# Optimization experiments

Measured on AMD Instinct MI355X. Metric: run time of the kernel, lower is better.

## Reference

```python
import jax, jax.numpy as jnp
import numpy as np

CAPACITY_FACTOR = 1.0


def setup_inputs() -> dict:
    key = jax.random.key(0)
    k1, k2, k3 = jax.random.split(key, 3)
    x = jax.random.normal(k1, (4, 2048, 2048), jnp.float32)          # [B, S, d_model]
    wg = jax.random.normal(k2, (2048, 8), jnp.float32) * 0.02        # gate weight [d_model, E]
    we = jax.random.normal(k3, (8, 2048, 8192), jnp.float32) * 0.02  # expert weights [E, d_model, d_ff]
    be = jnp.zeros((8, 8192), jnp.float32)                           # expert bias [E, d_ff]
    return {"x": x, "wg": wg, "we": we, "be": be}


def reference(x, wg, we, be):
    d = x.shape[-1]
    tokens = x.reshape(-1, d)                       # [S, d]  (S = total tokens)
    S = tokens.shape[0]
    E = wg.shape[1]
    C = int(S * CAPACITY_FACTOR) // E               # per-expert capacity

    # ---- top-1 gate (DeepSpeed-style) -> dispatch_mask [S, E, C] ----
    logits = tokens @ wg                            # [S, E]
    gates = jax.nn.softmax(logits, axis=-1)
    idx = jnp.argmax(gates, axis=-1)                # chosen expert per token
    mask1 = jax.nn.one_hot(idx, E, dtype=tokens.dtype)        # [S, E]
    locations = jnp.cumsum(mask1, axis=0) - 1.0               # position within expert queue
    mask1 = mask1 * (locations < C).astype(tokens.dtype)      # drop tokens over capacity
    loc_s = jnp.sum(locations * mask1, axis=1).astype(jnp.int32)  # [S]
    loc_oh = jax.nn.one_hot(loc_s, C, dtype=tokens.dtype)          # [S, C]
    dispatch_mask = mask1[:, :, None] * loc_oh[:, None, :]         # [S, E, C] one-hot

    # ---- dense one-hot dispatch: einsum('sec,sm->ecm') ----
    dispatched = jnp.einsum('sec,sm->ecm', dispatch_mask, tokens)  # [E, C, d]

    # AllToAll with ep_size=1 is identity; reshape (ep_size, num_local_experts, C, d)
    dispatched = dispatched.reshape(1, E, C, d)

    # ---- front experts: per-expert Linear (front half of FFN) ----
    out = jnp.einsum('gecd,edf->gecf', dispatched, we) + be[None, :, None, :]

    return out.reshape(-1, we.shape[-1])            # [E*C, d_ff]
```

## Files before the change

kernel.cpp:

```cpp
#include <hip/hip_runtime.h>
#include <hip/hip_bf16.h>

#define S_TOK 8192
#define DM    2048
#define DFF   8192
#define NE    8
#define CAP   1024

typedef __bf16 bf16_t;
typedef __bf16 bf16x8 __attribute__((ext_vector_type(8)));
typedef float  f32x4  __attribute__((ext_vector_type(4)));

__device__ __forceinline__ void load_lds16(const void* g, void* l) {
    __builtin_amdgcn_global_load_lds((const __attribute__((address_space(1))) void*)g,
                                     (__attribute__((address_space(3))) void*)l,
                                     16, 0, 0);
}

__global__ __launch_bounds__(256) void gate_argmax(const float* __restrict__ x,
                                                   const float* __restrict__ wg,
                                                   int* __restrict__ eidx) {
    int lane = threadIdx.x & 63, wv = threadIdx.x >> 6;
    int s = blockIdx.x * 4 + wv;
    const float* row = x + (size_t)s * DM;
    float acc[8] = {0.f,0.f,0.f,0.f,0.f,0.f,0.f,0.f};
    for (int kb = 0; kb < DM; kb += 256) {
        int k0 = kb + lane * 4;
        float4 xv = *(const float4*)(row + k0);
        const float* wr = wg + (size_t)k0 * NE;
        float xs[4] = {xv.x, xv.y, xv.z, xv.w};
#pragma unroll
        for (int c = 0; c < 4; ++c) {
            float4 w0 = *(const float4*)(wr + c * 8);
            float4 w1 = *(const float4*)(wr + c * 8 + 4);
            acc[0] += xs[c] * w0.x; acc[1] += xs[c] * w0.y;
            acc[2] += xs[c] * w0.z; acc[3] += xs[c] * w0.w;
            acc[4] += xs[c] * w1.x; acc[5] += xs[c] * w1.y;
            acc[6] += xs[c] * w1.z; acc[7] += xs[c] * w1.w;
        }
    }
#pragma unroll
    for (int off = 32; off > 0; off >>= 1)
#pragma unroll
        for (int e = 0; e < 8; ++e) acc[e] += __shfl_xor(acc[e], off, 64);
    if (lane == 0) {
        float best = acc[0]; int bi = 0;
#pragma unroll
        for (int e = 1; e < 8; ++e) if (acc[e] > best) { best = acc[e]; bi = e; }
        eidx[s] = bi;
    }
}

__global__ __launch_bounds__(64) void scatter_slots(const int* __restrict__ eidx,
                                                    int* __restrict__ srcOf) {
    int lane = threadIdx.x;
    unsigned long long below = (lane == 0) ? 0ull : ((1ull << lane) - 1ull);
    for (int i = lane; i < NE * CAP; i += 64) srcOf[i] = -1;

    int cnt[NE] = {0,0,0,0,0,0,0,0};
    int e_cur = eidx[lane];
    for (int it = 0; it < S_TOK / 64; ++it) {
        int e_nxt = (it < S_TOK / 64 - 1) ? eidx[(it + 1) * 64 + lane] : 0;
        int s = it * 64 + lane;
#pragma unroll
        for (int ex = 0; ex < NE; ++ex) {
            unsigned long long m = __ballot(e_cur == ex);
            if (e_cur == ex) {
                int loc = cnt[ex] + __popcll(m & below);
                if (loc < CAP) srcOf[ex * CAP + loc] = s;
            }
            cnt[ex] += __popcll(m);
        }
        e_cur = e_nxt;
    }
}

__global__ __launch_bounds__(256) void pack_rows(const float* __restrict__ x,
                                                 const int* __restrict__ srcOf,
                                                 char* __restrict__ abuf) {
    int slot = blockIdx.x;
    int e = slot >> 10, c = slot & 1023;
    int mt = c >> 8, m = c & 255;
    int src = srcOf[slot];
    int tid = threadIdx.x;
    int kt = tid >> 3, kg = tid & 7;
    bf16x8 v = {};
    if (src >= 0) {
        const float4* p = (const float4*)(x + (size_t)src * DM + kt * 64 + kg * 8);
        float4 a = p[0], b = p[1];
        v = bf16x8{(bf16_t)a.x,(bf16_t)a.y,(bf16_t)a.z,(bf16_t)a.w,
                   (bf16_t)b.x,(bf16_t)b.y,(bf16_t)b.z,(bf16_t)b.w};
    }
    size_t img = ((size_t)((e * 4 + mt) * 32 + kt)) << 15;
    int off = m * 128 + ((kg * 16) ^ ((m & 7) << 4));
    *(bf16x8*)(abuf + img + off) = v;
}

__global__ __launch_bounds__(512, 2) void moe_gemm(const char* __restrict__ abuf,
                                                   const float* __restrict__ we,
                                                   const float* __restrict__ be,
                                                   float* __restrict__ out) {
    __shared__ uint4 smem4[131072 / 16];
    char* smem = (char*)smem4;

    int bid = blockIdx.x;
    int e  = bid & 7;
    int r  = bid >> 3;
    int mt = r & 3;
    int nt = r >> 2;
    int tid = threadIdx.x, lane = tid & 63, wv = tid >> 6;
    int wm = wv >> 2, wn = wv & 3;
    int lr = lane & 15, g = lane >> 4;

    const char* aImg = abuf + (((size_t)((e * 4 + mt) * 32)) << 15);
    const float* bBase = we + (size_t)e * DM * DFF + (size_t)nt * 256 + lane * 4;
    int stOff = tid * 16;

    f32x4 acc[8][4] = {};
    float bs[16];

    auto issueB = [&](int kt, int h) {
        const float* bp = bBase + (size_t)(kt * 64 + wv * 8 + h * 4) * DFF;
#pragma unroll
        for (int j = 0; j < 4; ++j) {
            float4 t = *(const float4*)(bp + (size_t)j * DFF);
            bs[j * 4 + 0] = t.x; bs[j * 4 + 1] = t.y;
            bs[j * 4 + 2] = t.z; bs[j * 4 + 3] = t.w;
        }
    };
    auto issueA = [&](int kt, int buf) {
        const char* src = aImg + ((size_t)kt << 15) + stOff;
        char* dst = smem + buf * 65536 + stOff;
#pragma unroll
        for (int i = 0; i < 4; ++i) load_lds16(src + i * 8192, dst + i * 8192);
    };
    auto writeB = [&](int buf, int h) {
        char* bL = smem + buf * 65536 + 32768;
#pragma unroll
        for (int i = 0; i < 4; ++i) {
            int n = lane * 4 + i;
            ushort w[4];
#pragma unroll
            for (int j = 0; j < 4; ++j) {
                bf16_t b = (bf16_t)bs[j * 4 + i];
                w[j] = __builtin_bit_cast(unsigned short, b);
            }
            uint2 pk = { (unsigned)w[0] | ((unsigned)w[1] << 16),
                         (unsigned)w[2] | ((unsigned)w[3] << 16) };
            int slot = (n & 7) ^ ((n >> 3) & 7);
            *(uint2*)(bL + n * 128 + (((unsigned)(wv ^ slot)) << 4) + h * 8) = pk;
        }
    };

    issueA(0, 0);
    issueB(0, 0); writeB(0, 0);
    issueB(0, 1); writeB(0, 1);
    __syncthreads();

    int aRow = wm * 128 + lr;
    int bRow = wn * 64 + lr;
    int xa = lr & 7;

    for (int kt = 0; kt < 32; ++kt) {
        int cur = kt & 1, nxt = cur ^ 1;
        bool notlast = (kt < 31);
        const char* aC = smem + cur * 65536;
        const char* bC = aC + 32768;

        if (notlast) { issueA(kt + 1, nxt); issueB(kt + 1, 0); }
        __builtin_amdgcn_sched_barrier(0);

#pragma unroll
        for (int mh = 0; mh < 2; ++mh) {
            bf16x8 af[4][2];
#pragma unroll
            for (int mf = 0; mf < 4; ++mf) {
                int rowm = aRow + (mh * 4 + mf) * 16;
#pragma unroll
                for (int kk = 0; kk < 2; ++kk)
                    af[mf][kk] = *(const bf16x8*)(aC + rowm * 128 + (((kk * 4 + g) ^ xa) << 4));
            }
#pragma unroll
            for (int nh = 0; nh < 2; ++nh) {
                bf16x8 bfr[2][2];
#pragma unroll
                for (int nf = 0; nf < 2; ++nf) {
                    int rown = bRow + (nh * 2 + nf) * 16;
                    int xb = (rown & 7) ^ ((rown >> 3) & 7);
#pragma unroll
                    for (int kk = 0; kk < 2; ++kk)
                        bfr[nf][kk] = *(const bf16x8*)(bC + rown * 128 + (((kk * 4 + g) ^ xb) << 4));
                }
                __builtin_amdgcn_s_setprio(1);
#pragma unroll
                for (int mf = 0; mf < 4; ++mf)
#pragma unroll
                    for (int nf = 0; nf < 2; ++nf)
#pragma unroll
                        for (int kk = 0; kk < 2; ++kk)
                            acc[mh * 4 + mf][nh * 2 + nf] =
                                __builtin_amdgcn_mfma_f32_16x16x32_bf16(
                                    af[mf][kk], bfr[nf][kk],
                                    acc[mh * 4 + mf][nh * 2 + nf], 0, 0, 0);
                __builtin_amdgcn_s_setprio(0);
            }
            if (mh == 0 && notlast) { writeB(nxt, 0); issueB(kt + 1, 1); }
        }
        if (notlast) writeB(nxt, 1);
        __syncthreads();
    }

    int orow0 = e * CAP + mt * 256 + wm * 128 + g * 4;
    int ocol0 = nt * 256 + wn * 64 + lr;
#pragma unroll
    for (int nf = 0; nf < 4; ++nf) {
        int oc = ocol0 + nf * 16;
        float bias = be[(size_t)e * DFF + oc];
#pragma unroll
        for (int mf = 0; mf < 8; ++mf) {
            int orow = orow0 + mf * 16;
#pragma unroll
            for (int q = 0; q < 4; ++q)
                out[(size_t)(orow + q) * DFF + oc] = acc[mf][nf][q] + bias;
        }
    }
}

extern "C" void kernel_launch(void* const* d_in, const int* in_sizes, int n_in,
                              void* d_out, int out_size, void* d_ws, size_t ws_size,
                              hipStream_t stream) {
    const float* x  = (const float*)d_in[0];
    const float* wg = (const float*)d_in[1];
    const float* we = (const float*)d_in[2];
    const float* be = (const float*)d_in[3];
    float* out = (float*)d_out;

    size_t need = 65536 + (size_t)8 * 4 * 32 * 32768;
    if (ws_size < need) return;

    int* eidx  = (int*)d_ws;
    int* srcOf = eidx + S_TOK;
    char* abuf = (char*)d_ws + 65536;

    gate_argmax<<<S_TOK / 4, 256, 0, stream>>>(x, wg, eidx);
    scatter_slots<<<1, 64, 0, stream>>>(eidx, srcOf);
    pack_rows<<<S_TOK, 256, 0, stream>>>(x, srcOf, abuf);
    moe_gemm<<<NE * 4 * 32, 512, 0, stream>>>(abuf, we, be, out);
}
```

Baseline: 500.3 us.

## Restructure GEMM main loop into barrier-separated MFMA clusters with split B prefetch

Rewrites the moe_gemm k-loop as four explicit phases. Each phase loads its A/B fragments from LDS, then waits on lgkmcnt and a workgroup barrier, then runs an MFMA cluster. The next tile's B global loads are split into two register buffers so each half can be issued and written to LDS at different phases. The A fragments for the second M half are reused across both N halves. The goal is to interleave LDS reads, global prefetch and MFMAs across waves in a ping-pong style. The cost is many more s_barrier instructions per iteration and higher register pressure from keeping both B staging buffers live.

```diff
diff --git a/kernel.cpp b/kernel.cpp
--- a/kernel.cpp
+++ b/kernel.cpp
@@ -96,6 +96,24 @@
     *(bf16x8*)(abuf + img + off) = v;
 }
 
+#define CLUSTER(MH, NH)                                                              \
+    __builtin_amdgcn_s_setprio(1);                                                   \
+    _Pragma("unroll")                                                                \
+    for (int mf = 0; mf < 4; ++mf)                                                   \
+        _Pragma("unroll")                                                            \
+        for (int nf = 0; nf < 2; ++nf)                                               \
+            _Pragma("unroll")                                                        \
+            for (int kk = 0; kk < 2; ++kk)                                           \
+                acc[(MH)*4 + mf][(NH)*2 + nf] =                                      \
+                    __builtin_amdgcn_mfma_f32_16x16x32_bf16(                         \
+                        af[mf][kk], bfA[NH][nf][kk],                                 \
+                        acc[(MH)*4 + mf][(NH)*2 + nf], 0, 0, 0);                     \
+    __builtin_amdgcn_s_setprio(0);
+
+#define WAIT_LGKM0_SB()                                                              \
+    asm volatile("s_waitcnt lgkmcnt(0)" ::: "memory");                               \
+    __builtin_amdgcn_sched_barrier(0);
+
 __global__ __launch_bounds__(512, 2) void moe_gemm(const char* __restrict__ abuf,
                                                    const float* __restrict__ we,
                                                    const float* __restrict__ be,
@@ -117,24 +135,33 @@
     int stOff = tid * 16;
 
     f32x4 acc[8][4] = {};
-    float bs[16];
-
-    auto issueB = [&](int kt, int h) {
-        const float* bp = bBase + (size_t)(kt * 64 + wv * 8 + h * 4) * DFF;
-#pragma unroll
-        for (int j = 0; j < 4; ++j) {
-            float4 t = *(const float4*)(bp + (size_t)j * DFF);
-            bs[j * 4 + 0] = t.x; bs[j * 4 + 1] = t.y;
-            bs[j * 4 + 2] = t.z; bs[j * 4 + 3] = t.w;
-        }
-    };
+    float bs0[16], bs1[16];
+    bf16x8 af[4][2];
+    bf16x8 bfA[2][2][2];
+
     auto issueA = [&](int kt, int buf) {
         const char* src = aImg + ((size_t)kt << 15) + stOff;
         char* dst = smem + buf * 65536 + stOff;
 #pragma unroll
         for (int i = 0; i < 4; ++i) load_lds16(src + i * 8192, dst + i * 8192);
     };
-    auto writeB = [&](int buf, int h) {
+    auto issueB0 = [&](int kt) {
+        const float* bp = bBase + (size_t)(kt * 64 + wv * 8) * DFF;
+#pragma unroll
+        for (int j = 0; j < 4; ++j) {
+            float4 t = *(const float4*)(bp + (size_t)j * DFF);
+            bs0[j*4+0] = t.x; bs0[j*4+1] = t.y; bs0[j*4+2] = t.z; bs0[j*4+3] = t.w;
+        }
+    };
+    auto issueB1 = [&](int kt) {
+        const float* bp = bBase + (size_t)(kt * 64 + wv * 8 + 4) * DFF;
+#pragma unroll
+        for (int j = 0; j < 4; ++j) {
+            float4 t = *(const float4*)(bp + (size_t)j * DFF);
+            bs1[j*4+0] = t.x; bs1[j*4+1] = t.y; bs1[j*4+2] = t.z; bs1[j*4+3] = t.w;
+        }
+    };
+    auto writeB = [&](int buf, const float* bsv, int h) {
         char* bL = smem + buf * 65536 + 32768;
 #pragma unroll
         for (int i = 0; i < 4; ++i) {
@@ -142,7 +169,7 @@
             ushort w[4];
 #pragma unroll
             for (int j = 0; j < 4; ++j) {
-                bf16_t b = (bf16_t)bs[j * 4 + i];
+                bf16_t b = (bf16_t)bsv[j * 4 + i];
                 w[j] = __builtin_bit_cast(unsigned short, b);
             }
             uint2 pk = { (unsigned)w[0] | ((unsigned)w[1] << 16),
@@ -153,61 +180,71 @@
     };
 
     issueA(0, 0);
-    issueB(0, 0); writeB(0, 0);
-    issueB(0, 1); writeB(0, 1);
+    issueB0(0);
+    issueB1(0);
+    writeB(0, bs0, 0);
+    writeB(0, bs1, 1);
     __syncthreads();
 
-    int aRow = wm * 128 + lr;
-    int bRow = wn * 64 + lr;
-    int xa = lr & 7;
+    int aRowB = (wm * 128 + lr) * 128;
+    int colA[2] = { ((0 * 4 + g) ^ (lr & 7)) << 4, ((1 * 4 + g) ^ (lr & 7)) << 4 };
 
     for (int kt = 0; kt < 32; ++kt) {
         int cur = kt & 1, nxt = cur ^ 1;
-        bool notlast = (kt < 31);
+        bool nl = (kt < 31);
         const char* aC = smem + cur * 65536;
         const char* bC = aC + 32768;
 
-        if (notlast) { issueA(kt + 1, nxt); issueB(kt + 1, 0); }
-        __builtin_amdgcn_sched_barrier(0);
-
-#pragma unroll
-        for (int mh = 0; mh < 2; ++mh) {
-            bf16x8 af[4][2];
-#pragma unroll
-            for (int mf = 0; mf < 4; ++mf) {
-                int rowm = aRow + (mh * 4 + mf) * 16;
-#pragma unroll
-                for (int kk = 0; kk < 2; ++kk)
-                    af[mf][kk] = *(const bf16x8*)(aC + rowm * 128 + (((kk * 4 + g) ^ xa) << 4));
-            }
-#pragma unroll
-            for (int nh = 0; nh < 2; ++nh) {
-                bf16x8 bfr[2][2];
-#pragma unroll
-                for (int nf = 0; nf < 2; ++nf) {
-                    int rown = bRow + (nh * 2 + nf) * 16;
-                    int xb = (rown & 7) ^ ((rown >> 3) & 7);
-#pragma unroll
-                    for (int kk = 0; kk < 2; ++kk)
-                        bfr[nf][kk] = *(const bf16x8*)(bC + rown * 128 + (((kk * 4 + g) ^ xb) << 4));
-                }
-                __builtin_amdgcn_s_setprio(1);
-#pragma unroll
-                for (int mf = 0; mf < 4; ++mf)
-#pragma unroll
-                    for (int nf = 0; nf < 2; ++nf)
-#pragma unroll
-                        for (int kk = 0; kk < 2; ++kk)
-                            acc[mh * 4 + mf][nh * 2 + nf] =
-                                __builtin_amdgcn_mfma_f32_16x16x32_bf16(
-                                    af[mf][kk], bfr[nf][kk],
-                                    acc[mh * 4 + mf][nh * 2 + nf], 0, 0, 0);
-                __builtin_amdgcn_s_setprio(0);
-            }
-            if (mh == 0 && notlast) { writeB(nxt, 0); issueB(kt + 1, 1); }
-        }
-        if (notlast) writeB(nxt, 1);
-        __syncthreads();
+#pragma unroll
+        for (int mf = 0; mf < 4; ++mf) {
+            af[mf][0] = *(const bf16x8*)(aC + aRowB + mf * 2048 + colA[0]);
+            af[mf][1] = *(const bf16x8*)(aC + aRowB + mf * 2048 + colA[1]);
+        }
+#pragma unroll
+        for (int nf = 0; nf < 2; ++nf) {
+            int rowB = wn * 64 + nf * 16 + lr;
+            int xb = (lr & 7) ^ ((nf * 2 + (lr >> 3)) & 7);
+#pragma unroll
+            for (int kk = 0; kk < 2; ++kk)
+                bfA[0][nf][kk] = *(const bf16x8*)(bC + rowB * 128 + (((kk * 4 + g) ^ xb) << 4));
+        }
+        if (nl) { issueA(kt + 1, nxt); issueB0(kt + 1); }
+        __builtin_amdgcn_s_barrier();
+        WAIT_LGKM0_SB();
+        CLUSTER(0, 0);
+        __builtin_amdgcn_s_barrier();
+
+#pragma unroll
+        for (int nf = 0; nf < 2; ++nf) {
+            int rowB = wn * 64 + 32 + nf * 16 + lr;
+            int xb = (lr & 7) ^ ((4 + nf * 2 + (lr >> 3)) & 7);
+#pragma unroll
+            for (int kk = 0; kk < 2; ++kk)
+                bfA[1][nf][kk] = *(const bf16x8*)(bC + rowB * 128 + (((kk * 4 + g) ^ xb) << 4));
+        }
+        if (nl) issueB1(kt + 1);
+        __builtin_amdgcn_s_barrier();
+        WAIT_LGKM0_SB();
+        CLUSTER(0, 1);
+        __builtin_amdgcn_s_barrier();
+
+#pragma unroll
+        for (int mf = 0; mf < 4; ++mf) {
+            af[mf][0] = *(const bf16x8*)(aC + aRowB + 8192 + mf * 2048 + colA[0]);
+            af[mf][1] = *(const bf16x8*)(aC + aRowB + 8192 + mf * 2048 + colA[1]);
+        }
+        __builtin_amdgcn_s_barrier();
+        WAIT_LGKM0_SB();
+        CLUSTER(1, 0);
+        __builtin_amdgcn_s_barrier();
+
+        if (nl) writeB(nxt, bs0, 0);
+        __builtin_amdgcn_s_barrier();
+        WAIT_LGKM0_SB();
+        CLUSTER(1, 1);
+        if (nl) writeB(nxt, bs1, 1);
+        asm volatile("s_waitcnt lgkmcnt(0)" ::: "memory");
+        __builtin_amdgcn_s_barrier();
     }
 
     int orow0 = e * CAP + mt * 256 + wm * 128 + g * 4;
```

Result: slower. 553.1 us (+10.6%).

## Pre-convert expert weights to swizzled bf16 tiles and stream both operands via LDS DMA

Applied to the files above, without the earlier changes.

Adds a pass that converts the fp32 expert weights into pre-swizzled bf16 tile images in workspace. A new GEMM kernel then loads both A and B through global_load_lds into double-buffered LDS instead of having each thread read fp32 B and convert it on the fly. This takes the B conversion and register staging out of the GEMM main loop. The cost is an extra full read of the 512MB fp32 weights plus a 256MB bf16 write every call. The old path is kept as a fallback when the workspace is too small.

```diff
diff --git a/kernel.cpp b/kernel.cpp
--- a/kernel.cpp
+++ b/kernel.cpp
@@ -96,10 +96,30 @@
     *(bf16x8*)(abuf + img + off) = v;
 }
 
-__global__ __launch_bounds__(512, 2) void moe_gemm(const char* __restrict__ abuf,
-                                                   const float* __restrict__ we,
-                                                   const float* __restrict__ be,
-                                                   float* __restrict__ out) {
+__global__ __launch_bounds__(256) void convert_we(const float* __restrict__ we,
+                                                  char* __restrict__ bbuf) {
+    int blk = blockIdx.x;
+    int kt = blk & 31;
+    int ent = blk >> 5;
+    int nt = ent & 31, e = ent >> 5;
+    int n = threadIdx.x;
+    const float* src = we + ((size_t)e * DM + kt * 64) * DFF + nt * 256 + n;
+    char* dst = bbuf + ((size_t)blk << 15) + n * 128;
+    int xa = n & 7;
+#pragma unroll
+    for (int kg = 0; kg < 8; ++kg) {
+        bf16x8 v;
+#pragma unroll
+        for (int k8 = 0; k8 < 8; ++k8)
+            v[k8] = (bf16_t)src[(size_t)(kg * 8 + k8) * DFF];
+        *(bf16x8*)(dst + ((kg ^ xa) << 4)) = v;
+    }
+}
+
+__global__ __launch_bounds__(512, 2) void moe_gemm_bf16(const char* __restrict__ abuf,
+                                                        const char* __restrict__ bbuf,
+                                                        const float* __restrict__ be,
+                                                        float* __restrict__ out) {
     __shared__ uint4 smem4[131072 / 16];
     char* smem = (char*)smem4;
 
@@ -113,6 +133,110 @@
     int lr = lane & 15, g = lane >> 4;
 
     const char* aImg = abuf + (((size_t)((e * 4 + mt) * 32)) << 15);
+    const char* bImg = bbuf + (((size_t)((e * 32 + nt) * 32)) << 15);
+    int stOff = tid * 16;
+
+    f32x4 acc[8][4] = {};
+
+    auto issueA = [&](int kt, int buf) {
+        const char* src = aImg + ((size_t)kt << 15) + stOff;
+        char* dst = smem + buf * 65536 + stOff;
+#pragma unroll
+        for (int i = 0; i < 4; ++i) load_lds16(src + i * 8192, dst + i * 8192);
+    };
+    auto issueB = [&](int kt, int buf) {
+        const char* src = bImg + ((size_t)kt << 15) + stOff;
+        char* dst = smem + buf * 65536 + 32768 + stOff;
+#pragma unroll
+        for (int i = 0; i < 4; ++i) load_lds16(src + i * 8192, dst + i * 8192);
+    };
+
+    issueA(0, 0);
+    issueB(0, 0);
+    __syncthreads();
+
+    int aRowB = (wm * 128 + lr) * 128;
+    int xa = lr & 7;
+    int colA[2] = { ((0 * 4 + g) ^ xa) << 4, ((1 * 4 + g) ^ xa) << 4 };
+
+    for (int kt = 0; kt < 32; ++kt) {
+        int cur = kt & 1, nxt = cur ^ 1;
+        bool nl = (kt < 31);
+        const char* aC = smem + cur * 65536;
+        const char* bC = aC + 32768;
+
+        if (nl) { issueA(kt + 1, nxt); issueB(kt + 1, nxt); }
+        __builtin_amdgcn_sched_barrier(0);
+
+#pragma unroll
+        for (int mh = 0; mh < 2; ++mh) {
+            bf16x8 af[4][2];
+#pragma unroll
+            for (int mf = 0; mf < 4; ++mf) {
+                af[mf][0] = *(const bf16x8*)(aC + aRowB + mh * 8192 + mf * 2048 + colA[0]);
+                af[mf][1] = *(const bf16x8*)(aC + aRowB + mh * 8192 + mf * 2048 + colA[1]);
+            }
+#pragma unroll
+            for (int nh = 0; nh < 2; ++nh) {
+                bf16x8 bfr[2][2];
+#pragma unroll
+                for (int nf = 0; nf < 2; ++nf) {
+                    int rown = wn * 64 + nh * 32 + nf * 16 + lr;
+                    int xb = rown & 7;
+#pragma unroll
+                    for (int kk = 0; kk < 2; ++kk)
+                        bfr[nf][kk] = *(const bf16x8*)(bC + rown * 128 + (((kk * 4 + g) ^ xb) << 4));
+                }
+                __builtin_amdgcn_s_setprio(1);
+#pragma unroll
+                for (int mf = 0; mf < 4; ++mf)
+#pragma unroll
+                    for (int nf = 0; nf < 2; ++nf)
+#pragma unroll
+                        for (int kk = 0; kk < 2; ++kk)
+                            acc[mh * 4 + mf][nh * 2 + nf] =
+                                __builtin_amdgcn_mfma_f32_16x16x32_bf16(
+                                    af[mf][kk], bfr[nf][kk],
+                                    acc[mh * 4 + mf][nh * 2 + nf], 0, 0, 0);
+                __builtin_amdgcn_s_setprio(0);
+            }
+        }
+        __syncthreads();
+    }
+
+    int orow0 = e * CAP + mt * 256 + wm * 128 + g * 4;
+    int ocol0 = nt * 256 + wn * 64 + lr;
+#pragma unroll
+    for (int nf = 0; nf < 4; ++nf) {
+        int oc = ocol0 + nf * 16;
+        float bias = be[(size_t)e * DFF + oc];
+#pragma unroll
+        for (int mf = 0; mf < 8; ++mf) {
+            int orow = orow0 + mf * 16;
+#pragma unroll
+            for (int q = 0; q < 4; ++q)
+                out[(size_t)(orow + q) * DFF + oc] = acc[mf][nf][q] + bias;
+        }
+    }
+}
+
+__global__ __launch_bounds__(512, 2) void moe_gemm_f32b(const char* __restrict__ abuf,
+                                                        const float* __restrict__ we,
+                                                        const float* __restrict__ be,
+                                                        float* __restrict__ out) {
+    __shared__ uint4 smem4[131072 / 16];
+    char* smem = (char*)smem4;
+
+    int bid = blockIdx.x;
+    int e  = bid & 7;
+    int r  = bid >> 3;
+    int mt = r & 3;
+    int nt = r >> 2;
+    int tid = threadIdx.x, lane = tid & 63, wv = tid >> 6;
+    int wm = wv >> 2, wn = wv & 3;
+    int lr = lane & 15, g = lane >> 4;
+
+    const char* aImg = abuf + (((size_t)((e * 4 + mt) * 32)) << 15);
     const float* bBase = we + (size_t)e * DM * DFF + (size_t)nt * 256 + lane * 4;
     int stOff = tid * 16;
 
@@ -235,15 +359,23 @@
     const float* be = (const float*)d_in[3];
     float* out = (float*)d_out;
 
-    size_t need = 65536 + (size_t)8 * 4 * 32 * 32768;
-    if (ws_size < need) return;
+    size_t needSmall = 65536 + (size_t)32 * 1048576;
+    size_t needBig   = needSmall + (size_t)256 * 1048576;
+    if (ws_size < needSmall) return;
 
     int* eidx  = (int*)d_ws;
     int* srcOf = eidx + S_TOK;
     char* abuf = (char*)d_ws + 65536;
+    char* bbuf = abuf + (size_t)32 * 1048576;
 
     gate_argmax<<<S_TOK / 4, 256, 0, stream>>>(x, wg, eidx);
     scatter_slots<<<1, 64, 0, stream>>>(eidx, srcOf);
     pack_rows<<<S_TOK, 256, 0, stream>>>(x, srcOf, abuf);
-    moe_gemm<<<NE * 4 * 32, 512, 0, stream>>>(abuf, we, be, out);
-}
+
+    if (ws_size >= needBig) {
+        convert_we<<<NE * 32 * 32, 256, 0, stream>>>(we, bbuf);
+        moe_gemm_bf16<<<NE * 4 * 32, 512, 0, stream>>>(abuf, bbuf, be, out);
+    } else {
+        moe_gemm_f32b<<<NE * 4 * 32, 512, 0, stream>>>(abuf, we, be, out);
+    }
+}
```

Result: slower. 645.7 us (+29.1%).

## Split LDS tiles into halves and hand-schedule GEMM main loop with explicit waitcnts

Applied to the files above, without the earlier changes.

Repacks the A and B LDS images into two half-tiles indexed by the warp's m/n half, so each warp's fragments form a contiguous block. The main loop is rewritten as four MFMA clusters per k-step. Explicit s_waitcnt, s_barrier and sched_barrier calls interleave LDS fragment reads, global prefetch and B conversion writes with the MFMA clusters. The goal is to hide LDS and global latency behind MFMAs. The cost is more barriers per iteration and fragile hand-tuned wait counts.

```diff
diff --git a/kernel.cpp b/kernel.cpp
--- a/kernel.cpp
+++ b/kernel.cpp
@@ -92,7 +92,9 @@
                    (bf16_t)b.x,(bf16_t)b.y,(bf16_t)b.z,(bf16_t)b.w};
     }
     size_t img = ((size_t)((e * 4 + mt) * 32 + kt)) << 15;
-    int off = m * 128 + ((kg * 16) ^ ((m & 7) << 4));
+    int u = (m >> 6) & 1;
+    int pos = ((m >> 7) << 6) | (m & 63);
+    int off = u * 16384 + pos * 128 + ((kg * 16) ^ ((m & 7) << 4));
     *(bf16x8*)(abuf + img + off) = v;
 }
 
@@ -112,27 +114,31 @@
     int wm = wv >> 2, wn = wv & 3;
     int lr = lane & 15, g = lane >> 4;
 
-    const char* aImg = abuf + (((size_t)((e * 4 + mt) * 32)) << 15);
+    const char* aI = abuf + (((size_t)((e * 4 + mt) * 32)) << 15);
     const float* bBase = we + (size_t)e * DM * DFF + (size_t)nt * 256 + lane * 4;
     int stOff = tid * 16;
 
     f32x4 acc[8][4] = {};
-    float bs[16];
-
+    bf16x8 af[4][2];
+    bf16x8 bf0[2][2], bf1[2][2];
+    float  bs[16];
+
+    int colx[2] = { ((0 * 4 + g) ^ (lr & 7)) << 4, ((1 * 4 + g) ^ (lr & 7)) << 4 };
+    int posA = (wm * 64 + lr) * 128;
+
+    auto stageA = [&](int kt, int u) {
+        const char* src = aI + ((size_t)kt << 15) + u * 16384 + stOff;
+        char* dst = smem + (kt & 1) * 65536 + u * 16384 + stOff;
+        load_lds16(src, dst);
+        load_lds16(src + 8192, dst + 8192);
+    };
     auto issueB = [&](int kt, int h) {
         const float* bp = bBase + (size_t)(kt * 64 + wv * 8 + h * 4) * DFF;
 #pragma unroll
         for (int j = 0; j < 4; ++j) {
             float4 t = *(const float4*)(bp + (size_t)j * DFF);
-            bs[j * 4 + 0] = t.x; bs[j * 4 + 1] = t.y;
-            bs[j * 4 + 2] = t.z; bs[j * 4 + 3] = t.w;
-        }
-    };
-    auto issueA = [&](int kt, int buf) {
-        const char* src = aImg + ((size_t)kt << 15) + stOff;
-        char* dst = smem + buf * 65536 + stOff;
-#pragma unroll
-        for (int i = 0; i < 4; ++i) load_lds16(src + i * 8192, dst + i * 8192);
+            bs[j*4+0] = t.x; bs[j*4+1] = t.y; bs[j*4+2] = t.z; bs[j*4+3] = t.w;
+        }
     };
     auto writeB = [&](int buf, int h) {
         char* bL = smem + buf * 65536 + 32768;
@@ -147,67 +153,95 @@
             }
             uint2 pk = { (unsigned)w[0] | ((unsigned)w[1] << 16),
                          (unsigned)w[2] | ((unsigned)w[3] << 16) };
-            int slot = (n & 7) ^ ((n >> 3) & 7);
-            *(uint2*)(bL + n * 128 + (((unsigned)(wv ^ slot)) << 4) + h * 8) = pk;
+            int u = (n >> 5) & 1;
+            int pos = ((n >> 6) << 5) | (n & 31);
+            int swz = (n & 7) ^ ((n >> 3) & 7);
+            *(uint2*)(bL + u * 16384 + pos * 128 + (((unsigned)(wv ^ swz)) << 4) + h * 8) = pk;
         }
     };
 
-    issueA(0, 0);
-    issueB(0, 0); writeB(0, 0);
-    issueB(0, 1); writeB(0, 1);
-    __syncthreads();
-
-    int aRow = wm * 128 + lr;
-    int bRow = wn * 64 + lr;
-    int xa = lr & 7;
-
-    for (int kt = 0; kt < 32; ++kt) {
-        int cur = kt & 1, nxt = cur ^ 1;
-        bool notlast = (kt < 31);
-        const char* aC = smem + cur * 65536;
-        const char* bC = aC + 32768;
-
-        if (notlast) { issueA(kt + 1, nxt); issueB(kt + 1, 0); }
-        __builtin_amdgcn_sched_barrier(0);
-
-#pragma unroll
-        for (int mh = 0; mh < 2; ++mh) {
-            bf16x8 af[4][2];
-#pragma unroll
-            for (int mf = 0; mf < 4; ++mf) {
-                int rowm = aRow + (mh * 4 + mf) * 16;
-#pragma unroll
-                for (int kk = 0; kk < 2; ++kk)
-                    af[mf][kk] = *(const bf16x8*)(aC + rowm * 128 + (((kk * 4 + g) ^ xa) << 4));
-            }
-#pragma unroll
-            for (int nh = 0; nh < 2; ++nh) {
-                bf16x8 bfr[2][2];
-#pragma unroll
-                for (int nf = 0; nf < 2; ++nf) {
-                    int rown = bRow + (nh * 2 + nf) * 16;
-                    int xb = (rown & 7) ^ ((rown >> 3) & 7);
-#pragma unroll
-                    for (int kk = 0; kk < 2; ++kk)
-                        bfr[nf][kk] = *(const bf16x8*)(bC + rown * 128 + (((kk * 4 + g) ^ xb) << 4));
-                }
-                __builtin_amdgcn_s_setprio(1);
-#pragma unroll
-                for (int mf = 0; mf < 4; ++mf)
-#pragma unroll
-                    for (int nf = 0; nf < 2; ++nf)
-#pragma unroll
-                        for (int kk = 0; kk < 2; ++kk)
-                            acc[mh * 4 + mf][nh * 2 + nf] =
-                                __builtin_amdgcn_mfma_f32_16x16x32_bf16(
-                                    af[mf][kk], bfr[nf][kk],
-                                    acc[mh * 4 + mf][nh * 2 + nf], 0, 0, 0);
-                __builtin_amdgcn_s_setprio(0);
-            }
-            if (mh == 0 && notlast) { writeB(nxt, 0); issueB(kt + 1, 1); }
-        }
-        if (notlast) writeB(nxt, 1);
-        __syncthreads();
+#define RD_AF(U, TB)                                                                 \
+    _Pragma("unroll")                                                                \
+    for (int mf = 0; mf < 4; ++mf) {                                                 \
+        af[mf][0] = *(const bf16x8*)((TB) + (U)*16384 + posA + mf * 2048 + colx[0]); \
+        af[mf][1] = *(const bf16x8*)((TB) + (U)*16384 + posA + mf * 2048 + colx[1]); \
+    }
+#define RD_BF(DST, NH, TB)                                                           \
+    _Pragma("unroll")                                                                \
+    for (int nf = 0; nf < 2; ++nf) {                                                 \
+        int n_ = wn * 64 + (NH) * 32 + nf * 16 + lr;                                 \
+        int xb_ = (n_ & 7) ^ ((n_ >> 3) & 7);                                        \
+        int pb_ = (wn * 32 + nf * 16 + lr) * 128 + (NH) * 16384 + 32768;             \
+        DST[nf][0] = *(const bf16x8*)((TB) + pb_ + (((0 * 4 + g) ^ xb_) << 4));      \
+        DST[nf][1] = *(const bf16x8*)((TB) + pb_ + (((1 * 4 + g) ^ xb_) << 4));      \
+    }
+#define CLUSTER(MH, NH, BV)                                                          \
+    __builtin_amdgcn_s_setprio(1);                                                   \
+    _Pragma("unroll")                                                                \
+    for (int mf = 0; mf < 4; ++mf)                                                   \
+        _Pragma("unroll")                                                            \
+        for (int nf = 0; nf < 2; ++nf)                                               \
+            _Pragma("unroll")                                                        \
+            for (int kk = 0; kk < 2; ++kk)                                           \
+                acc[(MH)*4 + mf][(NH)*2 + nf] =                                      \
+                    __builtin_amdgcn_mfma_f32_16x16x32_bf16(                         \
+                        af[mf][kk], BV[nf][kk],                                      \
+                        acc[(MH)*4 + mf][(NH)*2 + nf], 0, 0, 0);                     \
+    __builtin_amdgcn_s_setprio(0);
+#define LGKM(N) asm volatile("s_waitcnt lgkmcnt(" #N ")" ::: "memory");              \
+                __builtin_amdgcn_sched_barrier(0);
+#define VMC(N)  asm volatile("s_waitcnt vmcnt(" #N ")" ::: "memory");                \
+                __builtin_amdgcn_sched_barrier(0);
+#define BARR()  __builtin_amdgcn_s_barrier(); __builtin_amdgcn_sched_barrier(0);
+
+    issueB(0, 0);
+    stageA(0, 0); stageA(0, 1);
+    VMC(4);
+    writeB(0, 0);
+    issueB(0, 1);
+    VMC(0);
+    writeB(0, 1);
+    LGKM(0);
+    BARR();
+    RD_AF(0, smem);
+
+    for (int t = 0; t < 32; ++t) {
+        const char* tb = smem + (t & 1) * 65536;
+        int nxt = (t + 1) & 1;
+        bool nl = (t < 31);
+
+        RD_BF(bf0, 0, tb);
+        RD_BF(bf1, 1, tb);
+        if (nl) {
+            issueB(t + 1, 0);
+            stageA(t + 1, 0); stageA(t + 1, 1);
+        }
+        BARR();
+        LGKM(4);
+        CLUSTER(0, 0, bf0);
+        BARR();
+
+        BARR();
+        LGKM(0);
+        CLUSTER(0, 1, bf1);
+        RD_AF(1, tb);
+        BARR();
+
+        VMC(4);
+        if (nl) { writeB(nxt, 0); issueB(t + 1, 1); }
+        BARR();
+        LGKM(4);
+        CLUSTER(1, 0, bf0);
+        VMC(4);
+        BARR();
+
+        VMC(0);
+        if (nl) writeB(nxt, 1);
+        BARR();
+        CLUSTER(1, 1, bf1);
+        LGKM(0);
+        if (nl) { RD_AF(0, smem + nxt * 65536); }
+        BARR();
     }
 
     int orow0 = e * CAP + mt * 256 + wm * 128 + g * 4;
@@ -224,6 +258,12 @@
                 out[(size_t)(orow + q) * DFF + oc] = acc[mf][nf][q] + bias;
         }
     }
+#undef RD_AF
+#undef RD_BF
+#undef CLUSTER
+#undef LGKM
+#undef VMC
+#undef BARR
 }
 
 extern "C" void kernel_launch(void* const* d_in, const int* in_sizes, int n_in,
@@ -235,7 +275,7 @@
     const float* be = (const float*)d_in[3];
     float* out = (float*)d_out;
 
-    size_t need = 65536 + (size_t)8 * 4 * 32 * 32768;
+    size_t need = 65536 + (size_t)32 * 1048576;
     if (ws_size < need) return;
 
     int* eidx  = (int*)d_ws;
```

Result: slower. 587.4 us (+17.4%).
